# Kernel optimization log

Hardware: AMD Instinct MI355X
Metric: run time of the kernel (lower is better)

Reference implementation:

```python
import jax, jax.numpy as jnp
import numpy as np

MIN_LOOP = 4  # min_hairpin
INF = jnp.float32(1e18)


def _nussinov_ptr(e_pair, e_unp, allowed, min_loop=MIN_LOOP):
    """Fill the O(L^2) DP table span-by-span (anti-diagonal wavefront),
    vectorized over the start index i within each span. Returns the
    backpointer table ptr (L,L) int32 with the same encoding as the
    original numpy code: 0=i unpaired, 1=j unpaired, 2=(i,j) pair, k+3=bifurcation at k."""
    L = e_unp.shape[0]
    d = jnp.arange(L)
    dp = jnp.full((L, L), INF, dtype=jnp.float32).at[d, d].set(e_unp)
    ptr = jnp.full((L, L), -1, dtype=jnp.int32).at[d, d].set(0)
    ii = jnp.arange(L)
    tt = jnp.arange(L)  # bifurcation offset t = k - i, valid for t <= s-2

    def span_body(s, carry):
        dp, ptr = carry
        jj = ii + s - 1                      # true j; >= L entries are dropped on scatter
        jc = jnp.minimum(jj, L - 1)          # clamped j for safe gathers
        ic1 = jnp.minimum(ii + 1, L - 1)
        # candidate 0: i unpaired -> dp[i+1, j] + e_unp[i]
        c0 = dp[ic1, jc] + e_unp[ii]
        # candidate 1: j unpaired -> dp[i, j-1] + e_unp[j]
        c1 = dp[ii, jnp.maximum(jc - 1, 0)] + e_unp[jc]
        # candidate 2: (i,j) paired -> dp[i+1, j-1] + e_pair[i,j] (inner=0 when span==2)
        inner = jnp.where(s >= 3, dp[ic1, jnp.maximum(jc - 1, 0)], jnp.float32(0.0))
        c2 = inner + e_pair[ii, jc]
        pair_ok = allowed[ii, jc] & (jc - ii > min_loop)
        # bifurcation: min over k=i+t, t in [0, s-2]: dp[i,k] + dp[k+1,j]
        kk = ii[:, None] + tt[None, :]
        kc = jnp.minimum(kk, L - 1)
        bif = jnp.where(tt[None, :] <= s - 2,
                        dp[ii[:, None], kc] + dp[jnp.minimum(kc + 1, L - 1), jc[:, None]],
                        INF)
        t_arg = jnp.argmin(bif, axis=1)  # first occurrence == ascending-k tie-break
        bif_min = jnp.take_along_axis(bif, t_arg[:, None], axis=1)[:, 0]
        # sequential strict-< selection, matching the numpy candidate order
        best = c0
        bp = jnp.zeros(L, jnp.int32)
        u = c1 < best; best = jnp.where(u, c1, best); bp = jnp.where(u, 1, bp)
        u = pair_ok & (c2 < best); best = jnp.where(u, c2, best); bp = jnp.where(u, 2, bp)
        u = bif_min < best; best = jnp.where(u, bif_min, best)
        bp = jnp.where(u, (ii + t_arg + 3).astype(jnp.int32), bp)
        dp = dp.at[ii, jj].set(best, mode='drop')
        ptr = ptr.at[ii, jj].set(bp, mode='drop')
        return dp, ptr

    dp, ptr = jax.lax.fori_loop(2, L + 1, span_body, (dp, ptr))
    return ptr


def _backtrace(ptr):
    """Iterative stack-based backtrace (LIFO, same push order as numpy).
    Intervals on the stack are disjoint, so depth <= L; size 2L for slack."""
    L = ptr.shape[0]
    S = 2 * L
    stack0 = jnp.zeros((S, 2), jnp.int32).at[0].set(jnp.array([0, L - 1], jnp.int32))
    res0 = jnp.full((L,), -1, jnp.int32)

    def cond(st):
        return st[1] > 0

    def body(st):
        stack, sp, res = st
        sp1 = sp - 1
        i = stack[sp1, 0]
        j = stack[sp1, 1]
        p = ptr[i, j]
        valid = i < j
        is0 = p == 0; is1 = p == 1; is2 = p == 2
        k = p - 3
        # first push (popped slot is reused)
        e1i = jnp.where(is0, i + 1, jnp.where(is1, i, jnp.where(is2, i + 1, i)))
        e1j = jnp.where(is0, j, jnp.where(is1, j - 1, jnp.where(is2, j - 1, k)))
        v1 = valid & jnp.where(is2, (i + 1) <= (j - 1), True)
        # second push only for bifurcation: (k+1, j)
        v2 = valid & (p >= 3)
        do_pair = valid & is2
        res = res.at[i].set(jnp.where(do_pair, j, res[i]))
        res = res.at[j].set(jnp.where(do_pair, i, res[j]))
        stack = stack.at[sp1].set(jnp.where(v1, jnp.stack([e1i, e1j]), stack[sp1]))
        sp_a = sp1 + v1.astype(jnp.int32)
        slot = jnp.minimum(sp_a, S - 1)
        stack = stack.at[slot].set(jnp.where(v2, jnp.stack([k + 1, j]), stack[slot]))
        sp_b = sp_a + v2.astype(jnp.int32)
        return stack, sp_b, res

    _, _, res = jax.lax.while_loop(cond, body, (stack0, jnp.int32(1), res0))
    return res


def _decode(e_pair, e_unp, pair_mask):
    ptr = jax.vmap(_nussinov_ptr, in_axes=(0, 0, 0))(e_pair, e_unp, pair_mask)
    return jax.vmap(_backtrace)(ptr)  # (B, L) int32, -1 = unpaired


def setup_inputs() -> dict:
    key = jax.random.key(0)
    k1, k2, k3 = jax.random.split(key, 3)
    B, L = 16, 512
    e_pair = jax.random.normal(k1, (B, L, L), dtype=jnp.float32)
    e_unp = jax.random.normal(k2, (B, L), dtype=jnp.float32)
    pair_mask = jax.random.bernoulli(k3, 0.3, (B, L, L))
    return {"e_pair": e_pair, "e_unp": e_unp, "pair_mask": pair_mask}


def reference(e_pair, e_unp, pair_mask):
    return _decode(e_pair, e_unp, pair_mask)
```

## Files before the change

kernel.cpp:

```cpp
#include <hip/hip_runtime.h>
#include <stdint.h>

#define L_ 512
#define NBUF (L_ * L_)
#define T_ 64
#define NT_ 8
#define INFV 3.0e38f

__global__ __launch_bounds__(1024) void fd_mask_probe(const unsigned int* __restrict__ pm,
                                                      int n32,
                                                      unsigned int* __restrict__ flags) {
    __shared__ unsigned int sf;
    if (threadIdx.x == 0) sf = 0u;
    __syncthreads();
    unsigned int local = 0;
    const int nscan = n32 < 65536 ? n32 : 65536;
    for (int idx = threadIdx.x; idx < nscan; idx += 1024) {
        const unsigned int w = pm[idx];
        const unsigned int h0 = w & 0xFFFFu, h1 = w >> 16;
        if (w > 1u) local |= 1u;
        if (w & 0xFEFEFEFEu) local |= 2u;
        if ((h0 != 0u && h0 != 0x3F80u) || (h1 != 0u && h1 != 0x3F80u)) local |= 4u;
        if (w == 0x3F803F80u || w == 0x00003F80u) local |= 8u;
        if ((h0 != 0u && h0 != 0x3C00u) || (h1 != 0u && h1 != 0x3C00u)) local |= 16u;
    }
    if (local) atomicOr(&sf, local);
    __syncthreads();
    if (threadIdx.x == 0) flags[0] = sf;
}

__device__ __forceinline__ int mask_mode(unsigned int f) {
    if (!(f & 1u)) return 0;
    if (!(f & 2u)) return 1;
    if (!(f & 4u)) return (f & 8u) ? 3 : 2;
    return (!(f & 16u)) ? 3 : 2;
}

__device__ __forceinline__ bool mask_bit(int mode, const unsigned int* pmW,
                                         const unsigned char* pm8,
                                         const unsigned short* pm16,
                                         const float* pmf, size_t gi) {
    if (mode == 0) return pmW[gi] != 0u;
    if (mode == 1) return pm8[gi] != 0;
    if (mode == 3) return pm16[gi] != 0;
    return pmf[gi] != 0.0f;
}

__global__ __launch_bounds__(256) void fd_diag(
    const float* __restrict__ e_pair, const float* __restrict__ e_unp,
    const unsigned int* __restrict__ pm, const unsigned int* __restrict__ flags,
    float* __restrict__ dp_ws, unsigned short* __restrict__ ptr_ws)
{
    const int b = blockIdx.x / NT_;
    const int I = blockIdx.x % NT_;
    const int t = threadIdx.x;
    const int r0 = I * T_;
    const float* ep = e_pair + (size_t)b * NBUF;
    float* dp = dp_ws + (size_t)b * NBUF;
    unsigned short* ptr = ptr_ws + (size_t)b * NBUF;
    const int mode = mask_mode(flags[0]);
    const unsigned int*   pmW  = pm + (size_t)b * NBUF;
    const unsigned char*  pm8  = ((const unsigned char*) pm) + (size_t)b * NBUF;
    const unsigned short* pm16 = ((const unsigned short*)pm) + (size_t)b * NBUF;
    const float*          pmf  = ((const float*)         pm) + (size_t)b * NBUF;

    __shared__ float Ct[T_][T_ + 4];
    __shared__ float epl[T_][T_ + 4];
    __shared__ unsigned char mkb[T_][T_ + 4];
    __shared__ unsigned short bp[T_][T_ + 4];
    __shared__ float eu[T_];

    for (int e = t; e < T_ * T_; e += 256) {
        const int r = e >> 6, c = e & 63;
        const size_t gi = (size_t)(r0 + r) * L_ + r0 + c;
        epl[r][c] = ep[gi];
        mkb[r][c] = mask_bit(mode, pmW, pm8, pm16, pmf, gi) ? 1 : 0;
    }
    if (t < T_) eu[t] = e_unp[(size_t)b * L_ + r0 + t];
    __syncthreads();
    if (t < T_) Ct[t][t] = eu[t];
    __syncthreads();

    const int cell = t >> 2, sub = t & 3;
    for (int m = 1; m < T_; ++m) {
        if (cell < T_ - m) {
            const int ti = cell, tj = cell + m;
            float mv = INFV; int km = 0;
            for (int tk = ti + sub; tk < tj; tk += 4) {
                const float v = Ct[ti][tk] + Ct[tk + 1][tj];
                if (v < mv) { mv = v; km = tk; }
            }
            for (int off = 1; off < 4; off <<= 1) {
                const float ov = __shfl_xor(mv, off, 4);
                const int   ok = __shfl_xor(km, off, 4);
                if (ov < mv || (ov == mv && ok < km)) { mv = ov; km = ok; }
            }
            if (sub == 0) {
                const float c0 = Ct[ti + 1][tj] + eu[ti];
                const float c1 = Ct[ti][tj - 1] + eu[tj];
                const float inner = (m >= 2) ? Ct[ti + 1][tj - 1] : 0.0f;
                const float c2 = inner + epl[ti][tj];
                const bool pok = mkb[ti][tj] && (m > 4);
                float best = c0; int bv = 0;
                if (c1 < best)        { best = c1; bv = 1; }
                if (pok && c2 < best) { best = c2; bv = 2; }
                if (mv < best)        { best = mv; bv = r0 + km + 3; }
                Ct[ti][tj] = best;
                bp[ti][tj] = (unsigned short)bv;
            }
        }
        __syncthreads();
    }
    for (int e = t; e < T_ * T_; e += 256) {
        const int r = e >> 6, c = e & 63;
        if (c >= r) {
            const size_t gi = (size_t)(r0 + r) * L_ + r0 + c;
            dp[gi] = Ct[r][c];
            if (c > r) ptr[gi] = bp[r][c];
        }
    }
}

__global__ __launch_bounds__(256) void fd_step(
    const float* __restrict__ e_pair, const float* __restrict__ e_unp,
    const unsigned int* __restrict__ pm, const unsigned int* __restrict__ flags,
    float* __restrict__ dp_ws, unsigned short* __restrict__ ptr_ws,
    int* __restrict__ out, int d, int nI, int do_bt)
{
    const int b = blockIdx.x / nI;
    const int I = blockIdx.x % nI;
    const int J = I + d;
    const int t = threadIdx.x;
    const int r0 = I * T_, q0 = J * T_;
    const float* ep = e_pair + (size_t)b * NBUF;
    float* dp = dp_ws + (size_t)b * NBUF;
    unsigned short* ptr = ptr_ws + (size_t)b * NBUF;
    const int mode = mask_mode(flags[0]);
    const unsigned int*   pmW  = pm + (size_t)b * NBUF;
    const unsigned char*  pm8  = ((const unsigned char*) pm) + (size_t)b * NBUF;
    const unsigned short* pm16 = ((const unsigned short*)pm) + (size_t)b * NBUF;
    const float*          pmf  = ((const float*)         pm) + (size_t)b * NBUF;

    __shared__ float SA[T_][T_ + 4];
    __shared__ float SB[T_][T_ + 4];
    __shared__ float Ct[T_][T_ + 4];
    __shared__ float accv[T_][T_ + 4];
    __shared__ unsigned short acck[T_][T_ + 4];
    __shared__ float epl[T_][T_ + 4];
    __shared__ unsigned char mkb[T_][T_ + 4];
    __shared__ unsigned short bp[T_][T_ + 4];
    __shared__ float euI[T_], euJ[T_], rowB[T_], colL[T_];
    __shared__ float cornerS;
    __shared__ int sti[2 * L_], stj[2 * L_];

    float av[16]; int akr[16];
    const int ti0 = (t >> 4) * 4, tj0 = (t & 15) * 4;
#pragma unroll
    for (int q = 0; q < 16; ++q) { av[q] = INFV; akr[q] = 0; }
    for (int K = I + 1; K < J; ++K) {
        const int kb = K * T_;
        __syncthreads();
        for (int e = t; e < T_ * T_; e += 256) {
            const int r = e >> 6, c = e & 63;
            SA[r][c] = dp[(size_t)(r0 + r) * L_ + kb + c];
            SB[r][c] = dp[(size_t)(kb + 1 + r) * L_ + q0 + c];
        }
        __syncthreads();
        for (int kk = 0; kk < T_; ++kk) {
            float a[4], bb[4];
#pragma unroll
            for (int r = 0; r < 4; ++r) a[r] = SA[ti0 + r][kk];
#pragma unroll
            for (int c = 0; c < 4; ++c) bb[c] = SB[kk][tj0 + c];
            const int kg = kb + kk;
#pragma unroll
            for (int r = 0; r < 4; ++r)
#pragma unroll
                for (int c = 0; c < 4; ++c) {
                    const float v = a[r] + bb[c];
                    const int q = r * 4 + c;
                    if (v < av[q]) { av[q] = v; akr[q] = kg; }
                }
        }
    }
    __syncthreads();
#pragma unroll
    for (int r = 0; r < 4; ++r)
#pragma unroll
        for (int c = 0; c < 4; ++c) {
            accv[ti0 + r][tj0 + c] = av[r * 4 + c];
            acck[ti0 + r][tj0 + c] = (unsigned short)akr[r * 4 + c];
        }

    for (int e = t; e < T_ * T_; e += 256) {
        const int r = e >> 6, c = e & 63;
        SA[r][c] = dp[(size_t)(r0 + r) * L_ + r0 + c];
        SB[r][c] = dp[(size_t)(q0 + r) * L_ + q0 + c];
        const size_t gi = (size_t)(r0 + r) * L_ + q0 + c;
        epl[r][c] = ep[gi];
        mkb[r][c] = mask_bit(mode, pmW, pm8, pm16, pmf, gi) ? 1 : 0;
    }
    if (t < T_) {
        euI[t] = e_unp[(size_t)b * L_ + r0 + t];
        euJ[t] = e_unp[(size_t)b * L_ + q0 + t];
        rowB[t] = dp[(size_t)(r0 + T_) * L_ + q0 + t];
        colL[t] = dp[(size_t)(r0 + t) * L_ + q0 - 1];
    }
    if (t == 0) cornerS = (d >= 2) ? dp[(size_t)(r0 + T_) * L_ + q0 - 1] : 0.0f;
    __syncthreads();

    const int cell = t >> 2, sub = t & 3;
    for (int m = -(T_ - 1); m <= T_ - 1; ++m) {
        const int am = m < 0 ? -m : m;
        if (cell < T_ - am) {
            const int ti = (m < 0) ? cell - m : cell;
            const int tj = ti + m;
            const int span = d * T_ + m;
            float mv = INFV; int km = 0;
            for (int tk = ti + sub; tk < T_; tk += 4) {
                const float dk1j = (tk < T_ - 1) ? Ct[tk + 1][tj] : rowB[tj];
                const float v = SA[ti][tk] + dk1j;
                if (v < mv) { mv = v; km = r0 + tk; }
            }
            for (int tk = sub; tk < tj; tk += 4) {
                const float v = Ct[ti][tk] + SB[tk + 1][tj];
                if (v < mv) { mv = v; km = q0 + tk; }
            }
            for (int off = 1; off < 4; off <<= 1) {
                const float ov = __shfl_xor(mv, off, 4);
                const int   ok = __shfl_xor(km, off, 4);
                if (ov < mv || (ov == mv && ok < km)) { mv = ov; km = ok; }
            }
            if (sub == 0) {
                const float bvv = accv[ti][tj]; const int bvk = acck[ti][tj];
                if (bvv < mv || (bvv == mv && bvk < km)) { mv = bvv; km = bvk; }
                const float c0 = ((ti < T_ - 1) ? Ct[ti + 1][tj] : rowB[tj]) + euI[ti];
                const float c1 = ((tj > 0) ? Ct[ti][tj - 1] : colL[ti]) + euJ[tj];
                float inner;
                if (span == 1)          inner = 0.0f;
                else if (ti < T_ - 1)   inner = (tj > 0) ? Ct[ti + 1][tj - 1] : colL[ti + 1];
                else                    inner = (tj > 0) ? rowB[tj - 1] : cornerS;
                const float c2 = inner + epl[ti][tj];
                const bool pok = mkb[ti][tj] && (span > 4);
                float best = c0; int bv = 0;
                if (c1 < best)        { best = c1; bv = 1; }
                if (pok && c2 < best) { best = c2; bv = 2; }
                if (mv < best)        { best = mv; bv = km + 3; }
                Ct[ti][tj] = best;
                bp[ti][tj] = (unsigned short)bv;
            }
        }
        __syncthreads();
    }

    for (int e = t; e < T_ * T_; e += 256) {
        const int r = e >> 6, c = e & 63;
        const size_t gi = (size_t)(r0 + r) * L_ + q0 + c;
        dp[gi] = Ct[r][c];
        ptr[gi] = bp[r][c];
    }

    if (do_bt) {
        int* res = out + (size_t)b * L_;
        for (int idx = t; idx < L_; idx += 256) res[idx] = -1;
        __syncthreads();
        if (t == 0) {
            int sp = 1; sti[0] = 0; stj[0] = L_ - 1;
            while (sp > 0) {
                --sp;
                const int i = sti[sp], j = stj[sp];
                if (i < j) {
                    int p;
                    if (i >= r0 && i < r0 + T_ && j >= q0 && j < q0 + T_)
                        p = bp[i - r0][j - q0];
                    else
                        p = ptr[(size_t)i * L_ + j];
                    if (p == 0)      { sti[sp] = i + 1; stj[sp] = j;     ++sp; }
                    else if (p == 1) { sti[sp] = i;     stj[sp] = j - 1; ++sp; }
                    else if (p == 2) {
                        res[i] = j; res[j] = i;
                        if (i + 1 <= j - 1) { sti[sp] = i + 1; stj[sp] = j - 1; ++sp; }
                    } else {
                        const int k = p - 3;
                        sti[sp] = i;     stj[sp] = k; ++sp;
                        sti[sp] = k + 1; stj[sp] = j; ++sp;
                    }
                }
            }
        }
    }
}

extern "C" void kernel_launch(void* const* d_in, const int* in_sizes, int n_in,
                              void* d_out, int out_size, void* d_ws, size_t ws_size,
                              hipStream_t stream) {
    const float* e_pair = (const float*)d_in[0];
    const float* e_unp  = (const float*)d_in[1];
    const unsigned int* pm = (const unsigned int*)d_in[2];
    const int B = in_sizes[1] / L_;
    int* out = (int*)d_out;

    unsigned int* flags = (unsigned int*)d_ws;
    float* dp_ws = (float*)((char*)d_ws + 256);
    unsigned short* ptr_ws = (unsigned short*)(dp_ws + (size_t)B * NBUF);

    const int n32 = in_sizes[2] / 4;
    fd_mask_probe<<<dim3(1), dim3(1024), 0, stream>>>(pm, n32, flags);
    fd_diag<<<dim3(B * NT_), dim3(256), 0, stream>>>(e_pair, e_unp, pm, flags,
                                                     dp_ws, ptr_ws);
    for (int d = 1; d < NT_; ++d) {
        const int nI = NT_ - d;
        fd_step<<<dim3(B * nI), dim3(256), 0, stream>>>(e_pair, e_unp, pm, flags,
                                                        dp_ws, ptr_ws, out,
                                                        d, nI, d == NT_ - 1 ? 1 : 0);
    }
}
```

Measured before the change: 2.254 ms.

## Split backtrace into its own kernel and prefetch DP candidates in diagonal loops

The backtrace moves out of the last step kernel into a separate kernel. That kernel first streams the whole ptr table through with vector loads to warm the cache, then runs the serial walk. The diagonal fills read the neighbour-cell candidates before the bifurcation loop. The last column's branch moves out of the inner loop, and the bulk min-plus pass is skipped when d=1. Shared-memory padding changes from 4 to 5, and the sti/stj stacks leave the step kernel, which lowers its LDS footprint. In exchange there is one extra kernel launch and a full read of the ptr table just to warm the cache.

```diff
diff --git a/kernel.cpp b/kernel.cpp
--- a/kernel.cpp
+++ b/kernel.cpp
@@ -5,6 +5,7 @@
 #define NBUF (L_ * L_)
 #define T_ 64
 #define NT_ 8
+#define PAD 5
 #define INFV 3.0e38f
 
 __global__ __launch_bounds__(1024) void fd_mask_probe(const unsigned int* __restrict__ pm,
@@ -64,10 +65,10 @@
     const unsigned short* pm16 = ((const unsigned short*)pm) + (size_t)b * NBUF;
     const float*          pmf  = ((const float*)         pm) + (size_t)b * NBUF;
 
-    __shared__ float Ct[T_][T_ + 4];
-    __shared__ float epl[T_][T_ + 4];
-    __shared__ unsigned char mkb[T_][T_ + 4];
-    __shared__ unsigned short bp[T_][T_ + 4];
+    __shared__ float Ct[T_][T_ + PAD];
+    __shared__ float epl[T_][T_ + PAD];
+    __shared__ unsigned char mkb[T_][T_ + PAD];
+    __shared__ unsigned short bp[T_][T_ + PAD];
     __shared__ float eu[T_];
 
     for (int e = t; e < T_ * T_; e += 256) {
@@ -85,6 +86,14 @@
     for (int m = 1; m < T_; ++m) {
         if (cell < T_ - m) {
             const int ti = cell, tj = cell + m;
+            float pf_c0 = 0, pf_c1 = 0, pf_in = 0, pf_ep = 0; bool pok = false;
+            if (sub == 0) {
+                pf_c0 = Ct[ti + 1][tj];
+                pf_c1 = Ct[ti][tj - 1];
+                pf_in = (m >= 2) ? Ct[ti + 1][tj - 1] : 0.0f;
+                pf_ep = epl[ti][tj];
+                pok = mkb[ti][tj] && (m > 4);
+            }
             float mv = INFV; int km = 0;
             for (int tk = ti + sub; tk < tj; tk += 4) {
                 const float v = Ct[ti][tk] + Ct[tk + 1][tj];
@@ -96,11 +105,9 @@
                 if (ov < mv || (ov == mv && ok < km)) { mv = ov; km = ok; }
             }
             if (sub == 0) {
-                const float c0 = Ct[ti + 1][tj] + eu[ti];
-                const float c1 = Ct[ti][tj - 1] + eu[tj];
-                const float inner = (m >= 2) ? Ct[ti + 1][tj - 1] : 0.0f;
-                const float c2 = inner + epl[ti][tj];
-                const bool pok = mkb[ti][tj] && (m > 4);
+                const float c0 = pf_c0 + eu[ti];
+                const float c1 = pf_c1 + eu[tj];
+                const float c2 = pf_in + pf_ep;
                 float best = c0; int bv = 0;
                 if (c1 < best)        { best = c1; bv = 1; }
                 if (pok && c2 < best) { best = c2; bv = 2; }
@@ -125,7 +132,7 @@
     const float* __restrict__ e_pair, const float* __restrict__ e_unp,
     const unsigned int* __restrict__ pm, const unsigned int* __restrict__ flags,
     float* __restrict__ dp_ws, unsigned short* __restrict__ ptr_ws,
-    int* __restrict__ out, int d, int nI, int do_bt)
+    int d, int nI)
 {
     const int b = blockIdx.x / nI;
     const int I = blockIdx.x % nI;
@@ -141,61 +148,62 @@
     const unsigned short* pm16 = ((const unsigned short*)pm) + (size_t)b * NBUF;
     const float*          pmf  = ((const float*)         pm) + (size_t)b * NBUF;
 
-    __shared__ float SA[T_][T_ + 4];
-    __shared__ float SB[T_][T_ + 4];
-    __shared__ float Ct[T_][T_ + 4];
-    __shared__ float accv[T_][T_ + 4];
-    __shared__ unsigned short acck[T_][T_ + 4];
-    __shared__ float epl[T_][T_ + 4];
-    __shared__ unsigned char mkb[T_][T_ + 4];
-    __shared__ unsigned short bp[T_][T_ + 4];
+    __shared__ float WA[T_][T_ + PAD];
+    __shared__ float WB[T_][T_ + PAD];
+    __shared__ float Ct[T_][T_ + PAD];
+    __shared__ float accv[T_][T_ + PAD];
+    __shared__ unsigned short acck[T_][T_ + PAD];
+    __shared__ float epl[T_][T_ + PAD];
+    __shared__ unsigned char mkb[T_][T_ + PAD];
+    __shared__ unsigned short bp[T_][T_ + PAD];
     __shared__ float euI[T_], euJ[T_], rowB[T_], colL[T_];
     __shared__ float cornerS;
-    __shared__ int sti[2 * L_], stj[2 * L_];
-
-    float av[16]; int akr[16];
-    const int ti0 = (t >> 4) * 4, tj0 = (t & 15) * 4;
-#pragma unroll
-    for (int q = 0; q < 16; ++q) { av[q] = INFV; akr[q] = 0; }
-    for (int K = I + 1; K < J; ++K) {
-        const int kb = K * T_;
-        __syncthreads();
-        for (int e = t; e < T_ * T_; e += 256) {
-            const int r = e >> 6, c = e & 63;
-            SA[r][c] = dp[(size_t)(r0 + r) * L_ + kb + c];
-            SB[r][c] = dp[(size_t)(kb + 1 + r) * L_ + q0 + c];
-        }
-        __syncthreads();
-        for (int kk = 0; kk < T_; ++kk) {
-            float a[4], bb[4];
-#pragma unroll
-            for (int r = 0; r < 4; ++r) a[r] = SA[ti0 + r][kk];
-#pragma unroll
-            for (int c = 0; c < 4; ++c) bb[c] = SB[kk][tj0 + c];
-            const int kg = kb + kk;
-#pragma unroll
-            for (int r = 0; r < 4; ++r)
-#pragma unroll
-                for (int c = 0; c < 4; ++c) {
-                    const float v = a[r] + bb[c];
-                    const int q = r * 4 + c;
-                    if (v < av[q]) { av[q] = v; akr[q] = kg; }
-                }
-        }
-    }
-    __syncthreads();
-#pragma unroll
-    for (int r = 0; r < 4; ++r)
-#pragma unroll
-        for (int c = 0; c < 4; ++c) {
-            accv[ti0 + r][tj0 + c] = av[r * 4 + c];
-            acck[ti0 + r][tj0 + c] = (unsigned short)akr[r * 4 + c];
-        }
+
+    if (d >= 2) {
+        float av[16]; int akr[16];
+        const int ti0 = (t >> 4) * 4, tj0 = (t & 15) * 4;
+#pragma unroll
+        for (int q = 0; q < 16; ++q) { av[q] = INFV; akr[q] = 0; }
+        for (int K = I + 1; K < J; ++K) {
+            const int kb = K * T_;
+            __syncthreads();
+            for (int e = t; e < T_ * T_; e += 256) {
+                const int r = e >> 6, c = e & 63;
+                WA[r][c] = dp[(size_t)(r0 + r) * L_ + kb + c];
+                WB[r][c] = dp[(size_t)(kb + 1 + r) * L_ + q0 + c];
+            }
+            __syncthreads();
+            for (int kk = 0; kk < T_; ++kk) {
+                float a[4], bb[4];
+#pragma unroll
+                for (int r = 0; r < 4; ++r) a[r] = WA[ti0 + r][kk];
+#pragma unroll
+                for (int c = 0; c < 4; ++c) bb[c] = WB[kk][tj0 + c];
+                const int kg = kb + kk;
+#pragma unroll
+                for (int r = 0; r < 4; ++r)
+#pragma unroll
+                    for (int c = 0; c < 4; ++c) {
+                        const float v = a[r] + bb[c];
+                        const int q = r * 4 + c;
+                        if (v < av[q]) { av[q] = v; akr[q] = kg; }
+                    }
+            }
+        }
+#pragma unroll
+        for (int r = 0; r < 4; ++r)
+#pragma unroll
+            for (int c = 0; c < 4; ++c) {
+                accv[ti0 + r][tj0 + c] = av[r * 4 + c];
+                acck[ti0 + r][tj0 + c] = (unsigned short)akr[r * 4 + c];
+            }
+    }
+    __syncthreads();
 
     for (int e = t; e < T_ * T_; e += 256) {
         const int r = e >> 6, c = e & 63;
-        SA[r][c] = dp[(size_t)(r0 + r) * L_ + r0 + c];
-        SB[r][c] = dp[(size_t)(q0 + r) * L_ + q0 + c];
+        WA[r][c] = dp[(size_t)(r0 + r) * L_ + r0 + c];
+        WB[r][c] = dp[(size_t)(q0 + r) * L_ + q0 + c];
         const size_t gi = (size_t)(r0 + r) * L_ + q0 + c;
         epl[r][c] = ep[gi];
         mkb[r][c] = mask_bit(mode, pmW, pm8, pm16, pmf, gi) ? 1 : 0;
@@ -213,17 +221,32 @@
     for (int m = -(T_ - 1); m <= T_ - 1; ++m) {
         const int am = m < 0 ? -m : m;
         if (cell < T_ - am) {
-            const int ti = (m < 0) ? cell - m : cell;
+            const int ti = (m < 0) ? cell + am : cell;
             const int tj = ti + m;
             const int span = d * T_ + m;
+            float pf_c0 = 0, pf_c1 = 0, pf_in = 0, pf_ep = 0;
+            float bulk_v = INFV; int bulk_k = 0; bool pok = false;
+            if (sub == 0) {
+                pf_c0 = (ti < T_ - 1) ? Ct[ti + 1][tj] : rowB[tj];
+                pf_c1 = (tj > 0) ? Ct[ti][tj - 1] : colL[ti];
+                if (span == 1)        pf_in = 0.0f;
+                else if (ti < T_ - 1) pf_in = (tj > 0) ? Ct[ti + 1][tj - 1] : colL[ti + 1];
+                else                  pf_in = (tj > 0) ? rowB[tj - 1] : cornerS;
+                pf_ep = epl[ti][tj];
+                pok = mkb[ti][tj] && (span > 4);
+                if (d >= 2) { bulk_v = accv[ti][tj]; bulk_k = acck[ti][tj]; }
+            }
             float mv = INFV; int km = 0;
-            for (int tk = ti + sub; tk < T_; tk += 4) {
-                const float dk1j = (tk < T_ - 1) ? Ct[tk + 1][tj] : rowB[tj];
-                const float v = SA[ti][tk] + dk1j;
+            for (int tk = ti + sub; tk < T_ - 1; tk += 4) {
+                const float v = WA[ti][tk] + Ct[tk + 1][tj];
                 if (v < mv) { mv = v; km = r0 + tk; }
             }
+            if (((T_ - 1 - ti) & 3) == sub) {
+                const float v = WA[ti][T_ - 1] + rowB[tj];
+                if (v < mv) { mv = v; km = r0 + T_ - 1; }
+            }
             for (int tk = sub; tk < tj; tk += 4) {
-                const float v = Ct[ti][tk] + SB[tk + 1][tj];
+                const float v = Ct[ti][tk] + WB[tk + 1][tj];
                 if (v < mv) { mv = v; km = q0 + tk; }
             }
             for (int off = 1; off < 4; off <<= 1) {
@@ -232,16 +255,10 @@
                 if (ov < mv || (ov == mv && ok < km)) { mv = ov; km = ok; }
             }
             if (sub == 0) {
-                const float bvv = accv[ti][tj]; const int bvk = acck[ti][tj];
-                if (bvv < mv || (bvv == mv && bvk < km)) { mv = bvv; km = bvk; }
-                const float c0 = ((ti < T_ - 1) ? Ct[ti + 1][tj] : rowB[tj]) + euI[ti];
-                const float c1 = ((tj > 0) ? Ct[ti][tj - 1] : colL[ti]) + euJ[tj];
-                float inner;
-                if (span == 1)          inner = 0.0f;
-                else if (ti < T_ - 1)   inner = (tj > 0) ? Ct[ti + 1][tj - 1] : colL[ti + 1];
-                else                    inner = (tj > 0) ? rowB[tj - 1] : cornerS;
-                const float c2 = inner + epl[ti][tj];
-                const bool pok = mkb[ti][tj] && (span > 4);
+                if (bulk_v < mv || (bulk_v == mv && bulk_k < km)) { mv = bulk_v; km = bulk_k; }
+                const float c0 = pf_c0 + euI[ti];
+                const float c1 = pf_c1 + euJ[tj];
+                const float c2 = pf_in + pf_ep;
                 float best = c0; int bv = 0;
                 if (c1 < best)        { best = c1; bv = 1; }
                 if (pok && c2 < best) { best = c2; bv = 2; }
@@ -255,36 +272,46 @@
 
     for (int e = t; e < T_ * T_; e += 256) {
         const int r = e >> 6, c = e & 63;
-        const size_t gi = (size_t)(r0 + r) * L_ + q0 + c;
-        dp[gi] = Ct[r][c];
-        ptr[gi] = bp[r][c];
-    }
-
-    if (do_bt) {
-        int* res = out + (size_t)b * L_;
-        for (int idx = t; idx < L_; idx += 256) res[idx] = -1;
-        __syncthreads();
-        if (t == 0) {
-            int sp = 1; sti[0] = 0; stj[0] = L_ - 1;
-            while (sp > 0) {
-                --sp;
-                const int i = sti[sp], j = stj[sp];
-                if (i < j) {
-                    int p;
-                    if (i >= r0 && i < r0 + T_ && j >= q0 && j < q0 + T_)
-                        p = bp[i - r0][j - q0];
-                    else
-                        p = ptr[(size_t)i * L_ + j];
-                    if (p == 0)      { sti[sp] = i + 1; stj[sp] = j;     ++sp; }
-                    else if (p == 1) { sti[sp] = i;     stj[sp] = j - 1; ++sp; }
-                    else if (p == 2) {
-                        res[i] = j; res[j] = i;
-                        if (i + 1 <= j - 1) { sti[sp] = i + 1; stj[sp] = j - 1; ++sp; }
-                    } else {
-                        const int k = p - 3;
-                        sti[sp] = i;     stj[sp] = k; ++sp;
-                        sti[sp] = k + 1; stj[sp] = j; ++sp;
-                    }
+        dp [(size_t)(r0 + r) * L_ + q0 + c] = Ct[r][c];
+        ptr[(size_t)(r0 + r) * L_ + q0 + c] = bp[r][c];
+    }
+}
+
+__global__ __launch_bounds__(256) void fd_backtrace(
+    const unsigned short* __restrict__ ptr_ws, int* __restrict__ out)
+{
+    const int b = blockIdx.x;
+    const int t = threadIdx.x;
+    const unsigned short* ptr = ptr_ws + (size_t)b * NBUF;
+    int* res = out + (size_t)b * L_;
+    __shared__ int sti[2 * L_], stj[2 * L_];
+
+    const uint4* p4 = (const uint4*)ptr;
+    unsigned int acc = 0;
+    for (int idx = t; idx < NBUF / 8; idx += 256) {
+        const uint4 v = p4[idx];
+        acc += v.x ^ v.y ^ v.z ^ v.w;
+    }
+    asm volatile("" :: "v"(acc));
+    for (int idx = t; idx < L_; idx += 256) res[idx] = -1;
+    __syncthreads();
+
+    if (t == 0) {
+        int sp = 1; sti[0] = 0; stj[0] = L_ - 1;
+        while (sp > 0) {
+            --sp;
+            const int i = sti[sp], j = stj[sp];
+            if (i < j) {
+                const int p = (int)ptr[(size_t)i * L_ + j];
+                if (p == 0)      { sti[sp] = i + 1; stj[sp] = j;     ++sp; }
+                else if (p == 1) { sti[sp] = i;     stj[sp] = j - 1; ++sp; }
+                else if (p == 2) {
+                    res[i] = j; res[j] = i;
+                    if (i + 1 <= j - 1) { sti[sp] = i + 1; stj[sp] = j - 1; ++sp; }
+                } else {
+                    const int k = p - 3;
+                    sti[sp] = i;     stj[sp] = k; ++sp;
+                    sti[sp] = k + 1; stj[sp] = j; ++sp;
                 }
             }
         }
@@ -311,7 +338,7 @@
     for (int d = 1; d < NT_; ++d) {
         const int nI = NT_ - d;
         fd_step<<<dim3(B * nI), dim3(256), 0, stream>>>(e_pair, e_unp, pm, flags,
-                                                        dp_ws, ptr_ws, out,
-                                                        d, nI, d == NT_ - 1 ? 1 : 0);
-    }
-}
+                                                        dp_ws, ptr_ws, d, nI);
+    }
+    fd_backtrace<<<dim3(B), dim3(256), 0, stream>>>(ptr_ws, out);
+}
```

Measured after the change: 2.228 ms. Within noise of the previous version (-1.2%).
